# Optimization experiments

Measured on AMD Instinct MI355X. Metric: run time of the kernel, lower is better.

Reference implementation:

```python
import jax, jax.numpy as jnp
import numpy as np

B, L = 32, 96
N = B * L
E = B * L * L
HID, LAT, EEMB = 128, 64, 32
NLAYERS = 3
LAMBDA_CONTRAST = 0.05


def _sinusoidal(t, dim):
    half = dim // 2
    freqs = jnp.exp(-jnp.log(10000.0) * jnp.arange(half, dtype=jnp.float32) / (half - 1))
    ang = t[:, None] * freqs[None, :]
    return jnp.concatenate([jnp.sin(ang), jnp.cos(ang)], axis=-1)


def _forward(H_0, X_0, H_1, X_1, cond_embedding, t_graph,
             Wi1, bi1, Wi2, bi2, Wi3, bi3, edge_table,
             We1, be1, We2, be2, Wx, Wh1, bh1, Wh2, bh2, Wout, bout,
             edges, chain_ids, generate_mask, lengths, shift):
    n = H_0.shape[0]
    b = lengths.shape[0]
    batch_ids = jnp.repeat(jnp.arange(b), lengths, total_repeat_length=n)
    t = t_graph[batch_ids]                      # (N,)
    mask = generate_mask
    mask_f = mask.astype(jnp.float32)

    # path interpolation
    tH = t[:, None]
    H_t = jnp.where(mask[:, None], (1.0 - tH) * H_0 + tH * H_1, H_1)
    X_t = jnp.where(mask[:, None], (1.0 - tH) * X_0 + tH * X_1, X_1)
    v_H_target = H_1 - H_0
    v_X_target = X_1 - X_0

    # edge types from chain-id masking (irregular gather)
    row, col = edges[0], edges[1]
    edge_types = (chain_ids[row] != chain_ids[col]).astype(jnp.int32)

    # --- velocity net ---
    t_embed = _sinusoidal(t, HID)
    h = jnp.concatenate([H_t, cond_embedding, t_embed], axis=-1)
    h = jax.nn.relu(h @ Wi1 + bi1)
    h = jax.nn.relu(h @ Wi2 + bi2)
    h = h @ Wi3 + bi3                            # (N, HID)
    eemb = edge_table[edge_types]                # (E, EEMB)

    X = X_t
    for l in range(NLAYERS):
        rel = X[row] - X[col]                    # (E, 3)
        d2 = jnp.sum(rel * rel, axis=-1, keepdims=True)
        ef = jnp.concatenate([h[row], h[col], d2, eemb], axis=-1)
        m = jax.nn.silu(ef @ We1[l] + be1[l])
        m = jax.nn.silu(m @ We2[l] + be2[l])     # (E, HID)
        coef = m @ Wx[l]                         # (E, 1)
        X = X + jax.ops.segment_sum(rel * coef, row, num_segments=n)
        agg = jax.ops.segment_sum(m, row, num_segments=n)
        hh = jnp.concatenate([h, agg], axis=-1)
        h = h + jax.nn.silu(hh @ Wh1[l] + bh1[l]) @ Wh2[l] + bh2[l]

    v_X_pred = jnp.where(mask[:, None], X, 0.0)
    v_H_pred = jnp.where(mask[:, None], h @ Wout + bout, 0.0)

    # --- losses ---
    msum = mask_f.sum() + 1e-8
    def masked_mse(pred, tgt):
        return (jnp.sum((pred - tgt) ** 2, axis=-1) * mask_f).sum() / msum
    loss_H_pos = masked_mse(v_H_pred, v_H_target)
    loss_X_pos = masked_mse(v_X_pred, v_X_target)

    # negatives: roll over node dim (matches torch indexing (arange+shift)%N)
    v_H_target_neg = jnp.roll(H_1, -shift, axis=0) - jnp.roll(H_0, -shift, axis=0)
    v_X_target_neg = jnp.roll(X_1, -shift, axis=0) - jnp.roll(X_0, -shift, axis=0)
    loss_H_neg = masked_mse(v_H_pred, v_H_target_neg)
    loss_X_neg = masked_mse(v_X_pred, v_X_target_neg)

    loss_H = loss_H_pos - LAMBDA_CONTRAST * loss_H_neg
    loss_X = loss_X_pos - LAMBDA_CONTRAST * loss_X_neg
    return jnp.stack([loss_H, loss_X, loss_H_pos, loss_X_pos, loss_H_neg, loss_X_neg])


def setup_inputs() -> dict:
    key = jax.random.key(0)
    ks = iter(jax.random.split(key, 40))
    def nrm(shape, fan_in):
        return jax.random.normal(next(ks), shape, dtype=jnp.float32) / np.sqrt(fan_in)

    # all-pairs edges within each graph (uniform lengths)
    idx = np.arange(L)
    rb, cb = np.repeat(idx, L), np.tile(idx, L)
    off = (np.arange(B) * L)[:, None]
    rows = (off + rb[None, :]).reshape(-1)
    cols = (off + cb[None, :]).reshape(-1)
    edges = jnp.asarray(np.stack([rows, cols]).astype(np.int32))

    d_in_mlp = LAT + 2 * HID       # 320
    d_in_e = 2 * HID + 1 + EEMB    # 289
    inp = {
        "H_0": jax.random.normal(next(ks), (N, LAT), dtype=jnp.float32),
        "X_0": jax.random.normal(next(ks), (N, 3), dtype=jnp.float32),
        "H_1": jax.random.normal(next(ks), (N, LAT), dtype=jnp.float32),
        "X_1": jax.random.normal(next(ks), (N, 3), dtype=jnp.float32),
        "cond_embedding": jax.random.normal(next(ks), (N, HID), dtype=jnp.float32),
        "t_graph": jax.random.uniform(next(ks), (B,), dtype=jnp.float32),
        "Wi1": nrm((d_in_mlp, HID), d_in_mlp), "bi1": jnp.zeros((HID,)),
        "Wi2": nrm((HID, HID), HID), "bi2": jnp.zeros((HID,)),
        "Wi3": nrm((HID, HID), HID), "bi3": jnp.zeros((HID,)),
        "edge_table": jax.random.normal(next(ks), (2, EEMB), dtype=jnp.float32),
        "We1": nrm((NLAYERS, d_in_e, HID), d_in_e), "be1": jnp.zeros((NLAYERS, HID)),
        "We2": nrm((NLAYERS, HID, HID), HID), "be2": jnp.zeros((NLAYERS, HID)),
        "Wx": nrm((NLAYERS, HID, 1), HID) * 0.01,
        "Wh1": nrm((NLAYERS, 2 * HID, HID), 2 * HID), "bh1": jnp.zeros((NLAYERS, HID)),
        "Wh2": nrm((NLAYERS, HID, HID), HID), "bh2": jnp.zeros((NLAYERS, HID)),
        "Wout": nrm((HID, LAT), HID), "bout": jnp.zeros((LAT,)),
        "edges": edges,
        "chain_ids": jax.random.randint(next(ks), (N,), 0, 3).astype(jnp.int32),
        "generate_mask": jax.random.bernoulli(next(ks), 0.5, (N,)),
        "lengths": jnp.full((B,), L, dtype=jnp.int32),
        "shift": 7,
    }
    return inp


def reference(H_0, X_0, H_1, X_1, cond_embedding, t_graph,
              Wi1, bi1, Wi2, bi2, Wi3, bi3, edge_table,
              We1, be1, We2, be2, Wx, Wh1, bh1, Wh2, bh2, Wout, bout,
              edges, chain_ids, generate_mask, lengths, shift):
    return _forward(H_0, X_0, H_1, X_1, cond_embedding, t_graph,
                    Wi1, bi1, Wi2, bi2, Wi3, bi3, edge_table,
                    We1, be1, We2, be2, Wx, Wh1, bh1, Wh2, bh2, Wout, bout,
                    edges, chain_ids, generate_mask, lengths, shift)
```

## Files before the change

kernel.cpp:

```cpp
#include <hip/hip_runtime.h>
#include <hip/hip_bf16.h>
#include <math.h>

#define NBATCH 32
#define LSEQ   96
#define NN     3072
#define HID    128
#define LAT    64
#define EEMB   32

#define OFF_H      0
#define OFF_X      (OFF_H   + NN*HID)
#define OFF_PA     (OFF_X   + NN*3)
#define OFF_AGG    (OFF_PA  + NN*HID)
#define OFF_DX     (OFF_AGG + NN*HID)
#define OFF_ET     (OFF_DX  + NN*3)
#define OFF_ACC    (OFF_ET  + 768)
#define OFF_NBID   (OFF_ACC + 8)
#define OFF_CUM    (OFF_NBID + NN)
#define OFF_PBH    (OFF_CUM + 40)
#define OFF_BPE    (OFF_PBH + NN*HID/2)
#define OFF_BAB    (OFF_BPE + 24576)
#define OFF_BH1    (OFF_BAB + 49152)
#define OFF_BH2    (OFF_BH1 + 49152)
#define OFF_BWO    (OFF_BH2 + 24576)
#define OFF_BWI1   (OFF_BWO + 4096)
#define OFF_BWI2   (OFF_BWI1 + 20480)
#define OFF_BWI3   (OFF_BWI2 + 8192)
#define OFF_CNT    (OFF_BWI3 + 8192)

typedef short bf16x8 __attribute__((ext_vector_type(8)));
typedef float f32x4  __attribute__((ext_vector_type(4)));

__device__ __forceinline__ short f2bf(float f) {
    unsigned u = __builtin_bit_cast(unsigned, f);
    unsigned r = (u + 0x7FFFu + ((u >> 16) & 1u)) >> 16;
    return (short)r;
}
__device__ __forceinline__ short2 f2bf2(float a, float b) {
    __hip_bfloat162 h = __float22bfloat162_rn(make_float2(a, b));
    short2 r;
    __builtin_memcpy(&r, &h, sizeof(r));
    return r;
}
__device__ __forceinline__ float bf2f(short s) {
    unsigned u = ((unsigned)(unsigned short)s) << 16;
    return __builtin_bit_cast(float, u);
}
__device__ __forceinline__ float silu(float z) {
    return z * __builtin_amdgcn_rcpf(1.0f + __expf(-z));
}

__global__ void k0_all(const float* __restrict__ edge_table, const float* __restrict__ We1,
                       const int* __restrict__ lengths, const float* __restrict__ We2,
                       const float* __restrict__ Wh1, const float* __restrict__ Wh2,
                       const float* __restrict__ Wout, const float* __restrict__ Wi1,
                       const float* __restrict__ Wi2, const float* __restrict__ Wi3,
                       float* __restrict__ ws) {
    int tid = threadIdx.x;
    if (blockIdx.x == 1472) {
        int* cum = (int*)(ws + OFF_CUM);
        int* nb  = (int*)(ws + OFF_NBID);
        float* et = ws + OFF_ET;
        if (tid == 0) {
            int s = 0;
            for (int b = 0; b < NBATCH; b++) { cum[b] = s; s += lengths[b]; }
            cum[NBATCH] = s;
        }
        if (tid < 8) ws[OFF_ACC + tid] = 0.0f;
        if (tid < 128) ((unsigned*)(ws + OFF_CNT))[tid] = 0u;
        __syncthreads();
        for (int i = tid; i < NN; i += blockDim.x) {
            int b = NBATCH - 1;
            for (int q = 0; q < NBATCH; q++) { if (i < cum[q + 1]) { b = q; break; } }
            nb[i] = b;
        }
        for (int idx = tid; idx < 3 * 2 * HID; idx += blockDim.x) {
            int c = idx & 127;
            int t = (idx >> 7) & 1;
            int l = idx >> 8;
            const float* w = We1 + (l * 289 + 257) * HID + c;
            const float* e = edge_table + t * EEMB;
            float s = 0.f;
            for (int k = 0; k < EEMB; k++) s += e[k] * w[k * HID];
            et[idx] = s;
        }
        return;
    }
    int idx = blockIdx.x * 256 + tid;
    short* bpe  = (short*)(ws + OFF_BPE);
    short* bab  = (short*)(ws + OFF_BAB);
    short* bh1  = (short*)(ws + OFF_BH1);
    short* bh2  = (short*)(ws + OFF_BH2);
    short* bwo  = (short*)(ws + OFF_BWO);
    short* bwi1 = (short*)(ws + OFF_BWI1);
    short* bwi2 = (short*)(ws + OFF_BWI2);
    short* bwi3 = (short*)(ws + OFF_BWI3);
    if (idx < 49152) {
        int k = idx & 127, n = (idx >> 7) & 127, l = idx >> 14;
        bpe[idx] = f2bf(We2[(l * 128 + k) * 128 + n]);
    } else if (idx < 147456) {
        int q = idx - 49152;
        int k = q & 127, n = (q >> 7) & 255, l = q >> 15;
        float v = (n < 128) ? We1[(l * 289 + k) * 128 + n]
                            : We1[(l * 289 + 128 + k) * 128 + (n - 128)];
        bab[q] = f2bf(v);
    } else if (idx < 245760) {
        int q = idx - 147456;
        int k = q & 255, n = (q >> 8) & 127, l = q >> 15;
        bh1[q] = f2bf(Wh1[(l * 256 + k) * 128 + n]);
    } else if (idx < 294912) {
        int q = idx - 245760;
        int k = q & 127, n = (q >> 7) & 127, l = q >> 14;
        bh2[q] = f2bf(Wh2[(l * 128 + k) * 128 + n]);
    } else if (idx < 303104) {
        int q = idx - 294912;
        int k = q & 127, n = q >> 7;
        bwo[q] = f2bf(Wout[k * 64 + n]);
    } else if (idx < 344064) {
        int q = idx - 303104;
        int n = q / 320, k = q - n * 320;
        bwi1[q] = f2bf(Wi1[k * 128 + n]);
    } else if (idx < 360448) {
        int q = idx - 344064;
        int k = q & 127, n = q >> 7;
        bwi2[q] = f2bf(Wi2[k * 128 + n]);
    } else if (idx < 376832) {
        int q = idx - 360448;
        int k = q & 127, n = q >> 7;
        bwi3[q] = f2bf(Wi3[k * 128 + n]);
    }
}

__global__ void __launch_bounds__(256)
k1s_node_init(const float* __restrict__ H0, const float* __restrict__ X0,
              const float* __restrict__ H1, const float* __restrict__ X1,
              const float* __restrict__ cond, const float* __restrict__ tg,
              const float* __restrict__ bi1, const float* __restrict__ bi2,
              const float* __restrict__ bi3, const float* __restrict__ be1,
              const int* __restrict__ gmask, float* __restrict__ ws) {
    __shared__ short u1[16 * 136];
    __shared__ short u2[16 * 136];
    int rowbase = blockIdx.x * 96 + blockIdx.y * 16;
    int tid = threadIdx.x;
    int w = tid >> 6, lane = tid & 63;
    int quad = lane >> 4, lp = lane & 15;
    int nodeA = rowbase + lp;
    const int* nb = (const int*)(ws + OFF_NBID);
    float t = tg[nb[nodeA]];
    float u = (gmask[nodeA] != 0) ? t : 1.0f;

    if (tid < 48) {
        int node = rowbase + tid / 3, d = tid % 3;
        float tn = tg[nb[node]];
        float un = (gmask[node] != 0) ? tn : 1.0f;
        ws[OFF_X + (size_t)node * 3 + d] =
            (1.0f - un) * X0[(size_t)node * 3 + d] + un * X1[(size_t)node * 3 + d];
    }

    const short* bwi1 = (const short*)(ws + OFF_BWI1);
    const short* bwi2 = (const short*)(ws + OFF_BWI2);
    const short* bwi3 = (const short*)(ws + OFF_BWI3);
    const short* bab  = (const short*)(ws + OFF_BAB);

    f32x4 acc[2];
    acc[0] = (f32x4){0.f, 0.f, 0.f, 0.f};
    acc[1] = (f32x4){0.f, 0.f, 0.f, 0.f};
    for (int s = 0; s < 10; s++) {
        int kb = s * 32 + quad * 8;
        float z[8];
        if (kb < 64) {
            const float* h0 = H0 + (size_t)nodeA * 64 + kb;
            const float* h1 = H1 + (size_t)nodeA * 64 + kb;
            #pragma unroll
            for (int e = 0; e < 8; e++) z[e] = (1.0f - u) * h0[e] + u * h1[e];
        } else if (kb < 192) {
            const float* cp = cond + (size_t)nodeA * 128 + (kb - 64);
            #pragma unroll
            for (int e = 0; e < 8; e++) z[e] = cp[e];
        } else if (kb < 256) {
            #pragma unroll
            for (int e = 0; e < 8; e++) {
                float c = (float)(kb - 192 + e);
                float fr = __expf(-9.2103403719761836f * c / 63.0f);
                z[e] = __sinf(t * fr);
            }
        } else {
            #pragma unroll
            for (int e = 0; e < 8; e++) {
                float c = (float)(kb - 256 + e);
                float fr = __expf(-9.2103403719761836f * c / 63.0f);
                z[e] = __cosf(t * fr);
            }
        }
        bf16x8 af;
        #pragma unroll
        for (int e = 0; e < 8; e += 2) {
            short2 p = f2bf2(z[e], z[e + 1]);
            af[e] = p.x; af[e + 1] = p.y;
        }
        #pragma unroll
        for (int i = 0; i < 2; i++) {
            int ct = 2 * w + i;
            bf16x8 bf = *(const bf16x8*)(bwi1 + (size_t)(16 * ct + lp) * 320 + kb);
            acc[i] = __builtin_amdgcn_mfma_f32_16x16x32_bf16(af, bf, acc[i], 0, 0, 0);
        }
    }
    #pragma unroll
    for (int i = 0; i < 2; i++) {
        int ch = 16 * (2 * w + i) + lp;
        float bb1 = bi1[ch];
        #pragma unroll
        for (int r = 0; r < 4; r++)
            u1[(quad * 4 + r) * 136 + ch] = f2bf(fmaxf(acc[i][r] + bb1, 0.0f));
    }
    __syncthreads();

    acc[0] = (f32x4){0.f, 0.f, 0.f, 0.f};
    acc[1] = (f32x4){0.f, 0.f, 0.f, 0.f};
    #pragma unroll
    for (int s = 0; s < 4; s++) {
        int kb = s * 32 + quad * 8;
        bf16x8 af = *(const bf16x8*)(u1 + lp * 136 + kb);
        #pragma unroll
        for (int i = 0; i < 2; i++) {
            int ct = 2 * w + i;
            bf16x8 bf = *(const bf16x8*)(bwi2 + (size_t)(16 * ct + lp) * 128 + kb);
            acc[i] = __builtin_amdgcn_mfma_f32_16x16x32_bf16(af, bf, acc[i], 0, 0, 0);
        }
    }
    #pragma unroll
    for (int i = 0; i < 2; i++) {
        int ch = 16 * (2 * w + i) + lp;
        float bb2 = bi2[ch];
        #pragma unroll
        for (int r = 0; r < 4; r++)
            u2[(quad * 4 + r) * 136 + ch] = f2bf(fmaxf(acc[i][r] + bb2, 0.0f));
    }
    __syncthreads();

    acc[0] = (f32x4){0.f, 0.f, 0.f, 0.f};
    acc[1] = (f32x4){0.f, 0.f, 0.f, 0.f};
    #pragma unroll
    for (int s = 0; s < 4; s++) {
        int kb = s * 32 + quad * 8;
        bf16x8 af = *(const bf16x8*)(u2 + lp * 136 + kb);
        #pragma unroll
        for (int i = 0; i < 2; i++) {
            int ct = 2 * w + i;
            bf16x8 bf = *(const bf16x8*)(bwi3 + (size_t)(16 * ct + lp) * 128 + kb);
            acc[i] = __builtin_amdgcn_mfma_f32_16x16x32_bf16(af, bf, acc[i], 0, 0, 0);
        }
    }
    #pragma unroll
    for (int i = 0; i < 2; i++) {
        int ch = 16 * (2 * w + i) + lp;
        float bb3 = bi3[ch];
        #pragma unroll
        for (int r = 0; r < 4; r++) {
            int row = quad * 4 + r;
            float h = acc[i][r] + bb3;
            ws[OFF_H + (size_t)(rowbase + row) * 128 + ch] = h;
            u1[row * 136 + ch] = f2bf(h);
        }
    }
    __syncthreads();

    f32x4 acc4[4];
    #pragma unroll
    for (int i = 0; i < 4; i++) acc4[i] = (f32x4){0.f, 0.f, 0.f, 0.f};
    #pragma unroll
    for (int s = 0; s < 4; s++) {
        int kb = s * 32 + quad * 8;
        bf16x8 af = *(const bf16x8*)(u1 + lp * 136 + kb);
        #pragma unroll
        for (int i = 0; i < 4; i++) {
            int ct4 = 4 * w + i;
            bf16x8 bf = *(const bf16x8*)(bab + (size_t)(16 * ct4 + lp) * 128 + kb);
            acc4[i] = __builtin_amdgcn_mfma_f32_16x16x32_bf16(af, bf, acc4[i], 0, 0, 0);
        }
    }
    short* pbh = (short*)(ws + OFF_PBH);
    #pragma unroll
    for (int i = 0; i < 4; i++) {
        int ct4 = 4 * w + i;
        #pragma unroll
        for (int r = 0; r < 4; r++) {
            int node = rowbase + quad * 4 + r;
            if (ct4 < 8) {
                int ch = 16 * ct4 + lp;
                ws[OFF_PA + (size_t)node * 128 + ch] = acc4[i][r] + be1[ch];
            } else {
                int ch = 16 * (ct4 - 8) + lp;
                pbh[(size_t)node * 128 + ch] = f2bf(acc4[i][r]);
            }
        }
    }
}

#define KG 4
#define SMC_BS    0
#define SMC_AGG   32768
#define SMC_PE0   45056
#define SMC_PE1   47104
#define SMC_WC    49152
#define SMC_BE2   49664
#define SMC_WX    50176
#define SMC_COEF  50688
#define SMC_XT    52224
#define SMC_CI    52272
__global__ void __launch_bounds__(384)
k3v_edge(const float* __restrict__ We1, const float* __restrict__ Wx,
         const float* __restrict__ be2, const int* __restrict__ chain,
         int l, float* __restrict__ ws) {
    __shared__ __align__(16) char smem[52288];
    short* bS    = (short*)(smem + SMC_BS);
    float* aggP  = (float*)(smem + SMC_AGG);
    float* pe0S  = (float*)(smem + SMC_PE0);
    float* pe1S  = (float*)(smem + SMC_PE1);
    float* wcS   = (float*)(smem + SMC_WC);
    float* be2S  = (float*)(smem + SMC_BE2);
    float* wxS   = (float*)(smem + SMC_WX);
    float* coefS = (float*)(smem + SMC_COEF);
    float* xT    = (float*)(smem + SMC_XT);
    int*   ciS   = (int*)  (smem + SMC_CI);

    int tid = threadIdx.x;
    int i0 = blockIdx.x * KG;
    int colbase = (i0 / 96) * 96;
    const float* Xc = ws + OFF_X;

    {
        const short* bpe = (const short*)(ws + OFF_BPE) + (size_t)l * 128 * 128;
        for (int idx = tid; idx < 2048; idx += 384) {
            int t = idx >> 8, s = (idx >> 6) & 3, ln = idx & 63;
            int lq = ln >> 4, lpp = ln & 15;
            *(bf16x8*)(bS + idx * 8) =
                *(const bf16x8*)(bpe + (size_t)(16 * t + lpp) * 128 + s * 32 + lq * 8);
        }
        if (tid < 128) {
            float et0 = ws[OFF_ET + l * 256 + tid];
            float et1 = ws[OFF_ET + l * 256 + 128 + tid];
            #pragma unroll
            for (int g = 0; g < KG; g++) {
                float pav = ws[OFF_PA + (size_t)(i0 + g) * 128 + tid];
                pe0S[g * 128 + tid] = pav + et0;
                pe1S[g * 128 + tid] = pav + et1;
            }
            wcS[tid]  = We1[(l * 289 + 256) * 128 + tid];
            be2S[tid] = be2[l * 128 + tid];
            wxS[tid]  = Wx[l * 128 + tid];
        }
        if (tid < KG * 3) xT[tid] = Xc[(size_t)(i0 + tid / 3) * 3 + tid % 3];
        if (tid < KG) ciS[tid] = chain[i0 + tid];
    }

    int w = tid >> 6, lane = tid & 63;
    int quad = lane >> 4, lp = lane & 15;
    int jA = 16 * w + lp;
    const short* pbrow = (const short*)(ws + OFF_PBH) + (size_t)(colbase + jA) * 128;
    float xr0 = Xc[(size_t)(colbase + jA) * 3 + 0];
    float xr1 = Xc[(size_t)(colbase + jA) * 3 + 1];
    float xr2 = Xc[(size_t)(colbase + jA) * 3 + 2];
    int cj = chain[colbase + jA];
    float ex0 = 0.f, ex1 = 0.f;
    if (w < 3) {
        ex0 = Xc[(size_t)(colbase + lane) * 3 + w];
        if (lane < 32) ex1 = Xc[(size_t)(colbase + lane + 64) * 3 + w];
    }
    __syncthreads();

    #pragma unroll
    for (int gr = 0; gr < 2; gr++) {
        int g0 = 2 * gr, g1 = 2 * gr + 1;
        float rx0 = xT[g0 * 3 + 0] - xr0, ry0 = xT[g0 * 3 + 1] - xr1, rz0 = xT[g0 * 3 + 2] - xr2;
        float rx1 = xT[g1 * 3 + 0] - xr0, ry1 = xT[g1 * 3 + 1] - xr1, rz1 = xT[g1 * 3 + 2] - xr2;
        float d20 = rx0 * rx0 + ry0 * ry0 + rz0 * rz0;
        float d21 = rx1 * rx1 + ry1 * ry1 + rz1 * rz1;
        const float* peB0 = ((cj != ciS[g0]) ? pe1S : pe0S) + g0 * 128;
        const float* peB1 = ((cj != ciS[g1]) ? pe1S : pe0S) + g1 * 128;

        bf16x8 af0[4], af1[4];
        #pragma unroll
        for (int s = 0; s < 4; s++) {
            int kb = s * 32 + quad * 8;
            bf16x8 pb = *(const bf16x8*)(pbrow + kb);
            float4 w0 = *(const float4*)(wcS + kb);
            float4 w1 = *(const float4*)(wcS + kb + 4);
            float wcv[8] = {w0.x, w0.y, w0.z, w0.w, w1.x, w1.y, w1.z, w1.w};
            float4 pa0 = *(const float4*)(peB0 + kb);
            float4 pa1 = *(const float4*)(peB0 + kb + 4);
            float4 pb0 = *(const float4*)(peB1 + kb);
            float4 pb1 = *(const float4*)(peB1 + kb + 4);
            float pe0v[8] = {pa0.x, pa0.y, pa0.z, pa0.w, pa1.x, pa1.y, pa1.z, pa1.w};
            float pe1v[8] = {pb0.x, pb0.y, pb0.z, pb0.w, pb1.x, pb1.y, pb1.z, pb1.w};
            float z0[8], z1[8];
            #pragma unroll
            for (int e = 0; e < 8; e++) {
                float pbf = bf2f(pb[e]);
                z0[e] = silu(pe0v[e] + pbf + d20 * wcv[e]);
                z1[e] = silu(pe1v[e] + pbf + d21 * wcv[e]);
            }
            #pragma unroll
            for (int e = 0; e < 8; e += 2) {
                short2 p0 = f2bf2(z0[e], z0[e + 1]);
                short2 p1 = f2bf2(z1[e], z1[e + 1]);
                af0[s][e] = p0.x; af0[s][e + 1] = p0.y;
                af1[s][e] = p1.x; af1[s][e + 1] = p1.y;
            }
        }

        float cp0[4] = {0.f, 0.f, 0.f, 0.f};
        float cp1[4] = {0.f, 0.f, 0.f, 0.f};
        #pragma unroll
        for (int t = 0; t < 8; t++) {
            f32x4 a0 = (f32x4){0.f, 0.f, 0.f, 0.f};
            f32x4 a1 = (f32x4){0.f, 0.f, 0.f, 0.f};
            #pragma unroll
            for (int s = 0; s < 4; s++) {
                bf16x8 bf = *(const bf16x8*)(bS + ((t * 4 + s) * 64 + lane) * 8);
                a0 = __builtin_amdgcn_mfma_f32_16x16x32_bf16(af0[s], bf, a0, 0, 0, 0);
                a1 = __builtin_amdgcn_mfma_f32_16x16x32_bf16(af1[s], bf, a1, 0, 0, 0);
            }
            float be2v = be2S[16 * t + lp];
            float wxv  = wxS[16 * t + lp];
            float ag0 = 0.f, ag1 = 0.f;
            #pragma unroll
            for (int r = 0; r < 4; r++) {
                float m20 = silu(a0[r] + be2v);
                float m21 = silu(a1[r] + be2v);
                ag0 += m20; ag1 += m21;
                cp0[r] += m20 * wxv;
                cp1[r] += m21 * wxv;
            }
            ag0 += __shfl_xor(ag0, 16); ag0 += __shfl_xor(ag0, 32);
            ag1 += __shfl_xor(ag1, 16); ag1 += __shfl_xor(ag1, 32);
            if (lane < 16) {
                aggP[(g0 * 6 + w) * 128 + 16 * t + lp] = ag0;
                aggP[(g1 * 6 + w) * 128 + 16 * t + lp] = ag1;
            }
        }
        #pragma unroll
        for (int r = 0; r < 4; r++) {
            float v0 = cp0[r], v1 = cp1[r];
            v0 += __shfl_xor(v0, 1); v1 += __shfl_xor(v1, 1);
            v0 += __shfl_xor(v0, 2); v1 += __shfl_xor(v1, 2);
            v0 += __shfl_xor(v0, 4); v1 += __shfl_xor(v1, 4);
            v0 += __shfl_xor(v0, 8); v1 += __shfl_xor(v1, 8);
            if (lp == 0) {
                coefS[g0 * 96 + 16 * w + quad * 4 + r] = v0;
                coefS[g1 * 96 + 16 * w + quad * 4 + r] = v1;
            }
        }
        __syncthreads();

        if (tid < 256) {
            int gg = tid >> 7, ch = tid & 127;
            int g = 2 * gr + gg;
            float s = 0.f;
            #pragma unroll
            for (int q = 0; q < 6; q++) s += aggP[(g * 6 + q) * 128 + ch];
            ws[OFF_AGG + (size_t)(i0 + g) * 128 + ch] = s;
        }
        if (w < 3) {
            #pragma unroll
            for (int gg = 0; gg < 2; gg++) {
                int g = 2 * gr + gg;
                float v = (xT[g * 3 + w] - ex0) * coefS[g * 96 + lane];
                if (lane < 32) v += (xT[g * 3 + w] - ex1) * coefS[g * 96 + lane + 64];
                #pragma unroll
                for (int o = 32; o > 0; o >>= 1) v += __shfl_down(v, o);
                if (lane == 0) ws[OFF_DX + (size_t)(i0 + g) * 3 + w] = v;
            }
        }
    }
}

__global__ void __launch_bounds__(256)
k4s_node_post(const float* __restrict__ bh1, const float* __restrict__ bh2,
              const float* __restrict__ be1, const float* __restrict__ bout,
              const float* __restrict__ H0, const float* __restrict__ X0,
              const float* __restrict__ H1, const float* __restrict__ X1,
              const int* __restrict__ gmask, const int* __restrict__ shiftp,
              int l, float* __restrict__ ws, float* __restrict__ out) {
    __shared__ short uS[16 * 136];
    __shared__ short hS[16 * 136];
    __shared__ float redE[4], redN[4];
    __shared__ float sxp, sxn, scnt;
    int rowbase = blockIdx.x * 96 + blockIdx.y * 16;
    int tid = threadIdx.x;
    int w = tid >> 6, lane = tid & 63;
    int quad = lane >> 4, lp = lane & 15;
    int nodeA = rowbase + lp;
    const short* b1 = (const short*)(ws + OFF_BH1) + (size_t)l * 128 * 256;
    const short* b2 = (const short*)(ws + OFF_BH2) + (size_t)l * 128 * 128;

    if (tid == 0) { sxp = 0.f; sxn = 0.f; scnt = 0.f; }
    if (tid < 48) {
        int node = rowbase + tid / 3, d = tid % 3;
        ws[OFF_X + (size_t)node * 3 + d] += ws[OFF_DX + (size_t)node * 3 + d];
    }

    f32x4 acc[2];
    acc[0] = (f32x4){0.f, 0.f, 0.f, 0.f};
    acc[1] = (f32x4){0.f, 0.f, 0.f, 0.f};
    #pragma unroll
    for (int s = 0; s < 8; s++) {
        int kb = s * 32 + quad * 8;
        const float* src = (kb < 128) ? (ws + OFF_H + (size_t)nodeA * 128 + kb)
                                      : (ws + OFF_AGG + (size_t)nodeA * 128 + (kb - 128));
        bf16x8 af;
        #pragma unroll
        for (int e = 0; e < 8; e += 2) {
            short2 p = f2bf2(src[e], src[e + 1]);
            af[e] = p.x; af[e + 1] = p.y;
        }
        #pragma unroll
        for (int i = 0; i < 2; i++) {
            int ct = 2 * w + i;
            bf16x8 bf = *(const bf16x8*)(b1 + (size_t)(16 * ct + lp) * 256 + kb);
            acc[i] = __builtin_amdgcn_mfma_f32_16x16x32_bf16(af, bf, acc[i], 0, 0, 0);
        }
    }
    #pragma unroll
    for (int i = 0; i < 2; i++) {
        int ch = 16 * (2 * w + i) + lp;
        float bb1 = bh1[l * 128 + ch];
        #pragma unroll
        for (int r = 0; r < 4; r++)
            uS[(quad * 4 + r) * 136 + ch] = f2bf(silu(acc[i][r] + bb1));
    }
    __syncthreads();

    acc[0] = (f32x4){0.f, 0.f, 0.f, 0.f};
    acc[1] = (f32x4){0.f, 0.f, 0.f, 0.f};
    #pragma unroll
    for (int s = 0; s < 4; s++) {
        int kb = s * 32 + quad * 8;
        bf16x8 af = *(const bf16x8*)(uS + lp * 136 + kb);
        #pragma unroll
        for (int i = 0; i < 2; i++) {
            int ct = 2 * w + i;
            bf16x8 bf = *(const bf16x8*)(b2 + (size_t)(16 * ct + lp) * 128 + kb);
            acc[i] = __builtin_amdgcn_mfma_f32_16x16x32_bf16(af, bf, acc[i], 0, 0, 0);
        }
    }
    #pragma unroll
    for (int i = 0; i < 2; i++) {
        int ch = 16 * (2 * w + i) + lp;
        float bb2 = bh2[l * 128 + ch];
        #pragma unroll
        for (int r = 0; r < 4; r++) {
            int row = quad * 4 + r;
            size_t off = OFF_H + (size_t)(rowbase + row) * 128 + ch;
            float h = ws[off] + acc[i][r] + bb2;
            ws[off] = h;
            hS[row * 136 + ch] = f2bf(h);
        }
    }
    __syncthreads();

    if (l < 2) {
        const short* bab = (const short*)(ws + OFF_BAB) + (size_t)(l + 1) * 256 * 128;
        f32x4 acc4[4];
        #pragma unroll
        for (int i = 0; i < 4; i++) acc4[i] = (f32x4){0.f, 0.f, 0.f, 0.f};
        #pragma unroll
        for (int s = 0; s < 4; s++) {
            int kb = s * 32 + quad * 8;
            bf16x8 af = *(const bf16x8*)(hS + lp * 136 + kb);
            #pragma unroll
            for (int i = 0; i < 4; i++) {
                int ct4 = 4 * w + i;
                bf16x8 bf = *(const bf16x8*)(bab + (size_t)(16 * ct4 + lp) * 128 + kb);
                acc4[i] = __builtin_amdgcn_mfma_f32_16x16x32_bf16(af, bf, acc4[i], 0, 0, 0);
            }
        }
        short* pbh = (short*)(ws + OFF_PBH);
        #pragma unroll
        for (int i = 0; i < 4; i++) {
            int ct4 = 4 * w + i;
            #pragma unroll
            for (int r = 0; r < 4; r++) {
                int node = rowbase + quad * 4 + r;
                if (ct4 < 8) {
                    int ch = 16 * ct4 + lp;
                    ws[OFF_PA + (size_t)node * 128 + ch] = acc4[i][r] + be1[(l + 1) * 128 + ch];
                } else {
                    int ch = 16 * (ct4 - 8) + lp;
                    pbh[(size_t)node * 128 + ch] = f2bf(acc4[i][r]);
                }
            }
        }
    } else {
        const short* bwo = (const short*)(ws + OFF_BWO);
        f32x4 accv = (f32x4){0.f, 0.f, 0.f, 0.f};
        #pragma unroll
        for (int s = 0; s < 4; s++) {
            int kb = s * 32 + quad * 8;
            bf16x8 af = *(const bf16x8*)(hS + lp * 136 + kb);
            bf16x8 bf = *(const bf16x8*)(bwo + (size_t)(16 * w + lp) * 128 + kb);
            accv = __builtin_amdgcn_mfma_f32_16x16x32_bf16(af, bf, accv, 0, 0, 0);
        }
        int s = shiftp[0] % NN; if (s < 0) s += NN;
        int col = 16 * w + lp;
        float bo = bout[col];
        float ep = 0.f, en = 0.f;
        #pragma unroll
        for (int r = 0; r < 4; r++) {
            int row = rowbase + quad * 4 + r;
            if (gmask[row] != 0) {
                int ip = row + s; if (ip >= NN) ip -= NN;
                float v  = accv[r] + bo;
                float tp = H1[(size_t)row * 64 + col] - H0[(size_t)row * 64 + col];
                float tn = H1[(size_t)ip * 64 + col]  - H0[(size_t)ip * 64 + col];
                float dp = v - tp, dn = v - tn;
                ep += dp * dp;
                en += dn * dn;
            }
        }
        #pragma unroll
        for (int o = 1; o < 64; o <<= 1) {
            ep += __shfl_xor(ep, o);
            en += __shfl_xor(en, o);
        }
        if (lane == 0) { redE[w] = ep; redN[w] = en; }

        if (tid < 16) {
            int node = rowbase + tid;
            if (gmask[node] != 0) {
                int ip = node + s; if (ip >= NN) ip -= NN;
                float xp = 0.f, xn = 0.f;
                #pragma unroll
                for (int d = 0; d < 3; d++) {
                    float xv  = ws[OFF_X + (size_t)node * 3 + d];
                    float tpx = X1[(size_t)node * 3 + d] - X0[(size_t)node * 3 + d];
                    float tnx = X1[(size_t)ip * 3 + d]   - X0[(size_t)ip * 3 + d];
                    xp += (xv - tpx) * (xv - tpx);
                    xn += (xv - tnx) * (xv - tnx);
                }
                atomicAdd(&sxp, xp);
                atomicAdd(&sxn, xn);
                atomicAdd(&scnt, 1.0f);
            }
        }
        __syncthreads();
        if (tid == 0) {
            float eT = redE[0] + redE[1] + redE[2] + redE[3];
            float nT = redN[0] + redN[1] + redN[2] + redN[3];
            float* acc0 = ws + OFF_ACC;
            atomicAdd(acc0 + 0, eT);
            atomicAdd(acc0 + 2, nT);
            atomicAdd(acc0 + 1, sxp);
            atomicAdd(acc0 + 3, sxn);
            atomicAdd(acc0 + 4, scnt);
            __threadfence();
            unsigned o2 = atomicAdd((unsigned*)(ws + OFF_CNT) + 96, 1u);
            if (o2 == 191u) {
                __threadfence();
                float a0 = atomicAdd(acc0 + 0, 0.0f);
                float a1 = atomicAdd(acc0 + 1, 0.0f);
                float a2 = atomicAdd(acc0 + 2, 0.0f);
                float a3 = atomicAdd(acc0 + 3, 0.0f);
                float a4 = atomicAdd(acc0 + 4, 0.0f);
                float msum = a4 + 1e-8f;
                float lhp = a0 / msum, lxp = a1 / msum;
                float lhn = a2 / msum, lxn = a3 / msum;
                out[0] = lhp - 0.05f * lhn;
                out[1] = lxp - 0.05f * lxn;
                out[2] = lhp;
                out[3] = lxp;
                out[4] = lhn;
                out[5] = lxn;
            }
        }
    }
}

extern "C" void kernel_launch(void* const* d_in, const int* in_sizes, int n_in,
                              void* d_out, int out_size, void* d_ws, size_t ws_size,
                              hipStream_t stream) {
    (void)in_sizes; (void)n_in; (void)out_size; (void)ws_size;
    const float* H0   = (const float*)d_in[0];
    const float* X0   = (const float*)d_in[1];
    const float* H1   = (const float*)d_in[2];
    const float* X1   = (const float*)d_in[3];
    const float* cond = (const float*)d_in[4];
    const float* tg   = (const float*)d_in[5];
    const float* Wi1  = (const float*)d_in[6];
    const float* bi1  = (const float*)d_in[7];
    const float* Wi2  = (const float*)d_in[8];
    const float* bi2  = (const float*)d_in[9];
    const float* Wi3  = (const float*)d_in[10];
    const float* bi3  = (const float*)d_in[11];
    const float* etab = (const float*)d_in[12];
    const float* We1  = (const float*)d_in[13];
    const float* be1  = (const float*)d_in[14];
    const float* We2  = (const float*)d_in[15];
    const float* be2  = (const float*)d_in[16];
    const float* Wx   = (const float*)d_in[17];
    const float* Wh1  = (const float*)d_in[18];
    const float* bh1  = (const float*)d_in[19];
    const float* Wh2  = (const float*)d_in[20];
    const float* bh2  = (const float*)d_in[21];
    const float* Wout = (const float*)d_in[22];
    const float* bout = (const float*)d_in[23];
    const int* chain   = (const int*)d_in[25];
    const int* gmask   = (const int*)d_in[26];
    const int* lengths = (const int*)d_in[27];
    const int* shiftp  = (const int*)d_in[28];
    float* ws  = (float*)d_ws;
    float* out = (float*)d_out;

    k0_all<<<1473, 256, 0, stream>>>(etab, We1, lengths, We2, Wh1, Wh2,
                                     Wout, Wi1, Wi2, Wi3, ws);
    k1s_node_init<<<dim3(NBATCH, 6), 256, 0, stream>>>(H0, X0, H1, X1, cond, tg,
                                                       bi1, bi2, bi3, be1, gmask, ws);
    for (int l = 0; l < 3; l++) {
        k3v_edge<<<NN / KG, 384, 0, stream>>>(We1, Wx, be2, chain, l, ws);
        k4s_node_post<<<dim3(NBATCH, 6), 256, 0, stream>>>(bh1, bh2, be1, bout,
                                                           H0, X0, H1, X1, gmask, shiftp,
                                                           l, ws, out);
    }
}
```

Before: 353.5 us.

## Read We2 fragments from global instead of LDS and halve nodes per edge block

The edge kernel no longer stages the 32 KB bf16 We2 tile in shared memory. Each MFMA B fragment is now loaded directly from global memory, where it should stay cache-resident. Each block handles 2 destination nodes instead of 4, so there are twice as many blocks and shared memory drops to about 10 KB. This is meant to raise occupancy and remove the per-block staging cost, at the price of repeated global/L2 reads of the weight fragments inside the MFMA loop.

```diff
diff --git a/kernel.cpp b/kernel.cpp
--- a/kernel.cpp
+++ b/kernel.cpp
@@ -298,67 +298,57 @@
     }
 }
 
-#define KG 4
-#define SMC_BS    0
-#define SMC_AGG   32768
-#define SMC_PE0   45056
-#define SMC_PE1   47104
-#define SMC_WC    49152
-#define SMC_BE2   49664
-#define SMC_WX    50176
-#define SMC_COEF  50688
-#define SMC_XT    52224
-#define SMC_CI    52272
+#define S2_AGG   0
+#define S2_PE0   6144
+#define S2_PE1   7168
+#define S2_WC    8192
+#define S2_BE2   8704
+#define S2_WX    9216
+#define S2_COEF  9728
+#define S2_XT    10496
+#define S2_CI    10520
 __global__ void __launch_bounds__(384)
-k3v_edge(const float* __restrict__ We1, const float* __restrict__ Wx,
+k3x_edge(const float* __restrict__ We1, const float* __restrict__ Wx,
          const float* __restrict__ be2, const int* __restrict__ chain,
          int l, float* __restrict__ ws) {
-    __shared__ __align__(16) char smem[52288];
-    short* bS    = (short*)(smem + SMC_BS);
-    float* aggP  = (float*)(smem + SMC_AGG);
-    float* pe0S  = (float*)(smem + SMC_PE0);
-    float* pe1S  = (float*)(smem + SMC_PE1);
-    float* wcS   = (float*)(smem + SMC_WC);
-    float* be2S  = (float*)(smem + SMC_BE2);
-    float* wxS   = (float*)(smem + SMC_WX);
-    float* coefS = (float*)(smem + SMC_COEF);
-    float* xT    = (float*)(smem + SMC_XT);
-    int*   ciS   = (int*)  (smem + SMC_CI);
+    __shared__ __align__(16) char smem[10528];
+    float* aggP  = (float*)(smem + S2_AGG);
+    float* pe0S  = (float*)(smem + S2_PE0);
+    float* pe1S  = (float*)(smem + S2_PE1);
+    float* wcS   = (float*)(smem + S2_WC);
+    float* be2S  = (float*)(smem + S2_BE2);
+    float* wxS   = (float*)(smem + S2_WX);
+    float* coefS = (float*)(smem + S2_COEF);
+    float* xT    = (float*)(smem + S2_XT);
+    int*   ciS   = (int*)  (smem + S2_CI);
 
     int tid = threadIdx.x;
-    int i0 = blockIdx.x * KG;
+    int i0 = blockIdx.x * 2;
     int colbase = (i0 / 96) * 96;
     const float* Xc = ws + OFF_X;
-
-    {
-        const short* bpe = (const short*)(ws + OFF_BPE) + (size_t)l * 128 * 128;
-        for (int idx = tid; idx < 2048; idx += 384) {
-            int t = idx >> 8, s = (idx >> 6) & 3, ln = idx & 63;
-            int lq = ln >> 4, lpp = ln & 15;
-            *(bf16x8*)(bS + idx * 8) =
-                *(const bf16x8*)(bpe + (size_t)(16 * t + lpp) * 128 + s * 32 + lq * 8);
-        }
-        if (tid < 128) {
-            float et0 = ws[OFF_ET + l * 256 + tid];
-            float et1 = ws[OFF_ET + l * 256 + 128 + tid];
-            #pragma unroll
-            for (int g = 0; g < KG; g++) {
-                float pav = ws[OFF_PA + (size_t)(i0 + g) * 128 + tid];
-                pe0S[g * 128 + tid] = pav + et0;
-                pe1S[g * 128 + tid] = pav + et1;
-            }
-            wcS[tid]  = We1[(l * 289 + 256) * 128 + tid];
-            be2S[tid] = be2[l * 128 + tid];
-            wxS[tid]  = Wx[l * 128 + tid];
-        }
-        if (tid < KG * 3) xT[tid] = Xc[(size_t)(i0 + tid / 3) * 3 + tid % 3];
-        if (tid < KG) ciS[tid] = chain[i0 + tid];
-    }
+    const short* bpe = (const short*)(ws + OFF_BPE) + (size_t)l * 128 * 128;
+
+    if (tid < 128) {
+        float et0 = ws[OFF_ET + l * 256 + tid];
+        float et1 = ws[OFF_ET + l * 256 + 128 + tid];
+        #pragma unroll
+        for (int g = 0; g < 2; g++) {
+            float pav = ws[OFF_PA + (size_t)(i0 + g) * 128 + tid];
+            pe0S[g * 128 + tid] = pav + et0;
+            pe1S[g * 128 + tid] = pav + et1;
+        }
+        wcS[tid]  = We1[(l * 289 + 256) * 128 + tid];
+        be2S[tid] = be2[l * 128 + tid];
+        wxS[tid]  = Wx[l * 128 + tid];
+    }
+    if (tid < 6) xT[tid] = Xc[(size_t)i0 * 3 + tid];
+    if (tid < 2) ciS[tid] = chain[i0 + tid];
 
     int w = tid >> 6, lane = tid & 63;
     int quad = lane >> 4, lp = lane & 15;
     int jA = 16 * w + lp;
     const short* pbrow = (const short*)(ws + OFF_PBH) + (size_t)(colbase + jA) * 128;
+    const short* bbase = bpe + (size_t)lp * 128 + quad * 8;
     float xr0 = Xc[(size_t)(colbase + jA) * 3 + 0];
     float xr1 = Xc[(size_t)(colbase + jA) * 3 + 1];
     float xr2 = Xc[(size_t)(colbase + jA) * 3 + 2];
@@ -370,108 +360,102 @@
     }
     __syncthreads();
 
-    #pragma unroll
-    for (int gr = 0; gr < 2; gr++) {
-        int g0 = 2 * gr, g1 = 2 * gr + 1;
-        float rx0 = xT[g0 * 3 + 0] - xr0, ry0 = xT[g0 * 3 + 1] - xr1, rz0 = xT[g0 * 3 + 2] - xr2;
-        float rx1 = xT[g1 * 3 + 0] - xr0, ry1 = xT[g1 * 3 + 1] - xr1, rz1 = xT[g1 * 3 + 2] - xr2;
-        float d20 = rx0 * rx0 + ry0 * ry0 + rz0 * rz0;
-        float d21 = rx1 * rx1 + ry1 * ry1 + rz1 * rz1;
-        const float* peB0 = ((cj != ciS[g0]) ? pe1S : pe0S) + g0 * 128;
-        const float* peB1 = ((cj != ciS[g1]) ? pe1S : pe0S) + g1 * 128;
-
-        bf16x8 af0[4], af1[4];
+    float rx0 = xT[0] - xr0, ry0 = xT[1] - xr1, rz0 = xT[2] - xr2;
+    float rx1 = xT[3] - xr0, ry1 = xT[4] - xr1, rz1 = xT[5] - xr2;
+    float d20 = rx0 * rx0 + ry0 * ry0 + rz0 * rz0;
+    float d21 = rx1 * rx1 + ry1 * ry1 + rz1 * rz1;
+    const float* peB0 = ((cj != ciS[0]) ? pe1S : pe0S);
+    const float* peB1 = ((cj != ciS[1]) ? pe1S : pe0S) + 128;
+
+    bf16x8 af0[4], af1[4];
+    #pragma unroll
+    for (int s = 0; s < 4; s++) {
+        int kb = s * 32 + quad * 8;
+        bf16x8 pb = *(const bf16x8*)(pbrow + kb);
+        float4 w0 = *(const float4*)(wcS + kb);
+        float4 w1 = *(const float4*)(wcS + kb + 4);
+        float wcv[8] = {w0.x, w0.y, w0.z, w0.w, w1.x, w1.y, w1.z, w1.w};
+        float4 pa0 = *(const float4*)(peB0 + kb);
+        float4 pa1 = *(const float4*)(peB0 + kb + 4);
+        float4 pb0 = *(const float4*)(peB1 + kb);
+        float4 pb1 = *(const float4*)(peB1 + kb + 4);
+        float pe0v[8] = {pa0.x, pa0.y, pa0.z, pa0.w, pa1.x, pa1.y, pa1.z, pa1.w};
+        float pe1v[8] = {pb0.x, pb0.y, pb0.z, pb0.w, pb1.x, pb1.y, pb1.z, pb1.w};
+        float z0[8], z1[8];
+        #pragma unroll
+        for (int e = 0; e < 8; e++) {
+            float pbf = bf2f(pb[e]);
+            z0[e] = silu(pe0v[e] + pbf + d20 * wcv[e]);
+            z1[e] = silu(pe1v[e] + pbf + d21 * wcv[e]);
+        }
+        #pragma unroll
+        for (int e = 0; e < 8; e += 2) {
+            short2 p0 = f2bf2(z0[e], z0[e + 1]);
+            short2 p1 = f2bf2(z1[e], z1[e + 1]);
+            af0[s][e] = p0.x; af0[s][e + 1] = p0.y;
+            af1[s][e] = p1.x; af1[s][e + 1] = p1.y;
+        }
+    }
+
+    float cp0[4] = {0.f, 0.f, 0.f, 0.f};
+    float cp1[4] = {0.f, 0.f, 0.f, 0.f};
+    #pragma unroll
+    for (int t = 0; t < 8; t++) {
+        f32x4 a0 = (f32x4){0.f, 0.f, 0.f, 0.f};
+        f32x4 a1 = (f32x4){0.f, 0.f, 0.f, 0.f};
         #pragma unroll
         for (int s = 0; s < 4; s++) {
-            int kb = s * 32 + quad * 8;
-            bf16x8 pb = *(const bf16x8*)(pbrow + kb);
-            float4 w0 = *(const float4*)(wcS + kb);
-            float4 w1 = *(const float4*)(wcS + kb + 4);
-            float wcv[8] = {w0.x, w0.y, w0.z, w0.w, w1.x, w1.y, w1.z, w1.w};
-            float4 pa0 = *(const float4*)(peB0 + kb);
-            float4 pa1 = *(const float4*)(peB0 + kb + 4);
-            float4 pb0 = *(const float4*)(peB1 + kb);
-            float4 pb1 = *(const float4*)(peB1 + kb + 4);
-            float pe0v[8] = {pa0.x, pa0.y, pa0.z, pa0.w, pa1.x, pa1.y, pa1.z, pa1.w};
-            float pe1v[8] = {pb0.x, pb0.y, pb0.z, pb0.w, pb1.x, pb1.y, pb1.z, pb1.w};
-            float z0[8], z1[8];
+            bf16x8 bf = *(const bf16x8*)(bbase + (size_t)t * 2048 + s * 32);
+            a0 = __builtin_amdgcn_mfma_f32_16x16x32_bf16(af0[s], bf, a0, 0, 0, 0);
+            a1 = __builtin_amdgcn_mfma_f32_16x16x32_bf16(af1[s], bf, a1, 0, 0, 0);
+        }
+        float be2v = be2S[16 * t + lp];
+        float wxv  = wxS[16 * t + lp];
+        float ag0 = 0.f, ag1 = 0.f;
+        #pragma unroll
+        for (int r = 0; r < 4; r++) {
+            float m20 = silu(a0[r] + be2v);
+            float m21 = silu(a1[r] + be2v);
+            ag0 += m20; ag1 += m21;
+            cp0[r] += m20 * wxv;
+            cp1[r] += m21 * wxv;
+        }
+        ag0 += __shfl_xor(ag0, 16); ag0 += __shfl_xor(ag0, 32);
+        ag1 += __shfl_xor(ag1, 16); ag1 += __shfl_xor(ag1, 32);
+        if (lane < 16) {
+            aggP[(0 * 6 + w) * 128 + 16 * t + lp] = ag0;
+            aggP[(1 * 6 + w) * 128 + 16 * t + lp] = ag1;
+        }
+    }
+    #pragma unroll
+    for (int r = 0; r < 4; r++) {
+        float v0 = cp0[r], v1 = cp1[r];
+        v0 += __shfl_xor(v0, 1); v1 += __shfl_xor(v1, 1);
+        v0 += __shfl_xor(v0, 2); v1 += __shfl_xor(v1, 2);
+        v0 += __shfl_xor(v0, 4); v1 += __shfl_xor(v1, 4);
+        v0 += __shfl_xor(v0, 8); v1 += __shfl_xor(v1, 8);
+        if (lp == 0) {
+            coefS[0 * 96 + 16 * w + quad * 4 + r] = v0;
+            coefS[1 * 96 + 16 * w + quad * 4 + r] = v1;
+        }
+    }
+    __syncthreads();
+
+    if (tid < 256) {
+        int gg = tid >> 7, ch = tid & 127;
+        float s = 0.f;
+        #pragma unroll
+        for (int q = 0; q < 6; q++) s += aggP[(gg * 6 + q) * 128 + ch];
+        ws[OFF_AGG + (size_t)(i0 + gg) * 128 + ch] = s;
+    }
+    if (w < 3) {
+        #pragma unroll
+        for (int gg = 0; gg < 2; gg++) {
+            float v = (xT[gg * 3 + w] - ex0) * coefS[gg * 96 + lane];
+            if (lane < 32) v += (xT[gg * 3 + w] - ex1) * coefS[gg * 96 + lane + 64];
             #pragma unroll
-            for (int e = 0; e < 8; e++) {
-                float pbf = bf2f(pb[e]);
-                z0[e] = silu(pe0v[e] + pbf + d20 * wcv[e]);
-                z1[e] = silu(pe1v[e] + pbf + d21 * wcv[e]);
-            }
-            #pragma unroll
-            for (int e = 0; e < 8; e += 2) {
-                short2 p0 = f2bf2(z0[e], z0[e + 1]);
-                short2 p1 = f2bf2(z1[e], z1[e + 1]);
-                af0[s][e] = p0.x; af0[s][e + 1] = p0.y;
-                af1[s][e] = p1.x; af1[s][e + 1] = p1.y;
-            }
-        }
-
-        float cp0[4] = {0.f, 0.f, 0.f, 0.f};
-        float cp1[4] = {0.f, 0.f, 0.f, 0.f};
-        #pragma unroll
-        for (int t = 0; t < 8; t++) {
-            f32x4 a0 = (f32x4){0.f, 0.f, 0.f, 0.f};
-            f32x4 a1 = (f32x4){0.f, 0.f, 0.f, 0.f};
-            #pragma unroll
-            for (int s = 0; s < 4; s++) {
-                bf16x8 bf = *(const bf16x8*)(bS + ((t * 4 + s) * 64 + lane) * 8);
-                a0 = __builtin_amdgcn_mfma_f32_16x16x32_bf16(af0[s], bf, a0, 0, 0, 0);
-                a1 = __builtin_amdgcn_mfma_f32_16x16x32_bf16(af1[s], bf, a1, 0, 0, 0);
-            }
-            float be2v = be2S[16 * t + lp];
-            float wxv  = wxS[16 * t + lp];
-            float ag0 = 0.f, ag1 = 0.f;
-            #pragma unroll
-            for (int r = 0; r < 4; r++) {
-                float m20 = silu(a0[r] + be2v);
-                float m21 = silu(a1[r] + be2v);
-                ag0 += m20; ag1 += m21;
-                cp0[r] += m20 * wxv;
-                cp1[r] += m21 * wxv;
-            }
-            ag0 += __shfl_xor(ag0, 16); ag0 += __shfl_xor(ag0, 32);
-            ag1 += __shfl_xor(ag1, 16); ag1 += __shfl_xor(ag1, 32);
-            if (lane < 16) {
-                aggP[(g0 * 6 + w) * 128 + 16 * t + lp] = ag0;
-                aggP[(g1 * 6 + w) * 128 + 16 * t + lp] = ag1;
-            }
-        }
-        #pragma unroll
-        for (int r = 0; r < 4; r++) {
-            float v0 = cp0[r], v1 = cp1[r];
-            v0 += __shfl_xor(v0, 1); v1 += __shfl_xor(v1, 1);
-            v0 += __shfl_xor(v0, 2); v1 += __shfl_xor(v1, 2);
-            v0 += __shfl_xor(v0, 4); v1 += __shfl_xor(v1, 4);
-            v0 += __shfl_xor(v0, 8); v1 += __shfl_xor(v1, 8);
-            if (lp == 0) {
-                coefS[g0 * 96 + 16 * w + quad * 4 + r] = v0;
-                coefS[g1 * 96 + 16 * w + quad * 4 + r] = v1;
-            }
-        }
-        __syncthreads();
-
-        if (tid < 256) {
-            int gg = tid >> 7, ch = tid & 127;
-            int g = 2 * gr + gg;
-            float s = 0.f;
-            #pragma unroll
-            for (int q = 0; q < 6; q++) s += aggP[(g * 6 + q) * 128 + ch];
-            ws[OFF_AGG + (size_t)(i0 + g) * 128 + ch] = s;
-        }
-        if (w < 3) {
-            #pragma unroll
-            for (int gg = 0; gg < 2; gg++) {
-                int g = 2 * gr + gg;
-                float v = (xT[g * 3 + w] - ex0) * coefS[g * 96 + lane];
-                if (lane < 32) v += (xT[g * 3 + w] - ex1) * coefS[g * 96 + lane + 64];
-                #pragma unroll
-                for (int o = 32; o > 0; o >>= 1) v += __shfl_down(v, o);
-                if (lane == 0) ws[OFF_DX + (size_t)(i0 + g) * 3 + w] = v;
-            }
+            for (int o = 32; o > 0; o >>= 1) v += __shfl_down(v, o);
+            if (lane == 0) ws[OFF_DX + (size_t)(i0 + gg) * 3 + w] = v;
         }
     }
 }
@@ -717,7 +701,7 @@
     k1s_node_init<<<dim3(NBATCH, 6), 256, 0, stream>>>(H0, X0, H1, X1, cond, tg,
                                                        bi1, bi2, bi3, be1, gmask, ws);
     for (int l = 0; l < 3; l++) {
-        k3v_edge<<<NN / KG, 384, 0, stream>>>(We1, Wx, be2, chain, l, ws);
+        k3x_edge<<<NN / 2, 384, 0, stream>>>(We1, Wx, be2, chain, l, ws);
         k4s_node_post<<<dim3(NBATCH, 6), 256, 0, stream>>>(bh1, bh2, be1, bout,
                                                            H0, X0, H1, X1, gmask, shiftp,
                                                            l, ws, out);
```

After: 390.7 us. 10.5% more time.
